# Optimization experiments

Hardware: AMD Instinct MI355X
Metric: run time of the kernel (lower is better)

## Reference

```python
import jax, jax.numpy as jnp
import numpy as np
import math

B, S, D, H, DFF = 4, 1024, 1024, 16, 4096
DK = D // H
EPS = 1e-5


def setup_inputs() -> dict:
    key = jax.random.key(0)
    ks = jax.random.split(key, 20)
    n = lambda k, shp: jax.random.normal(k, shp, jnp.float32) * 0.02
    inp = {
        "x": jax.random.normal(ks[0], (B, S, D), jnp.float32),
        "enc_output": jax.random.normal(ks[1], (B, S, D), jnp.float32),
        # source_mask is unused by the module's forward; target_mask is causal
        "source_mask": jnp.ones((B, 1, 1, S), jnp.int32),
        "target_mask": jnp.tril(jnp.ones((1, 1, S, S), jnp.int32)),
        # self-attention (torch Linear: y = x @ W.T + b)
        "sa_wq": n(ks[2], (D, D)), "sa_bq": jnp.zeros((D,), jnp.float32),
        "sa_wk": n(ks[3], (D, D)), "sa_bk": jnp.zeros((D,), jnp.float32),
        "sa_wv": n(ks[4], (D, D)), "sa_bv": jnp.zeros((D,), jnp.float32),
        "sa_wo": n(ks[5], (D, D)), "sa_bo": jnp.zeros((D,), jnp.float32),
        # cross-attention (nn.MultiheadAttention packed in_proj)
        "ca_in_w": n(ks[6], (3 * D, D)), "ca_in_b": jnp.zeros((3 * D,), jnp.float32),
        "ca_out_w": n(ks[7], (D, D)), "ca_out_b": jnp.zeros((D,), jnp.float32),
        # feed-forward
        "ff_w1": n(ks[8], (DFF, D)), "ff_b1": jnp.zeros((DFF,), jnp.float32),
        "ff_w2": n(ks[9], (D, DFF)), "ff_b2": jnp.zeros((D,), jnp.float32),
        # layer norms
        "n1_g": jnp.ones((D,), jnp.float32), "n1_b": jnp.zeros((D,), jnp.float32),
        "n2_g": jnp.ones((D,), jnp.float32), "n2_b": jnp.zeros((D,), jnp.float32),
        "n3_g": jnp.ones((D,), jnp.float32), "n3_b": jnp.zeros((D,), jnp.float32),
    }
    return inp


def _layernorm(x, g, b):
    m = jnp.mean(x, axis=-1, keepdims=True)
    v = jnp.var(x, axis=-1, keepdims=True)
    return (x - m) * jax.lax.rsqrt(v + EPS) * g + b


def _split_heads(t):  # [B,L,D] -> [B,H,L,DK]
    Bb, L, _ = t.shape
    return t.reshape(Bb, L, H, DK).transpose(0, 2, 1, 3)


def _attn(q, k, v, mask):
    # q,k,v: [B,H,Lq/ Lk, DK]
    scores = jnp.einsum("bhqd,bhkd->bhqk", q, k) / math.sqrt(DK)
    if mask is not None:
        scores = jnp.where(mask == 0, jnp.float32(-1e9), scores)
    probs = jax.nn.softmax(scores, axis=-1)
    out = jnp.einsum("bhqk,bhkd->bhqd", probs, v)  # [B,H,Lq,DK]
    Bb, _, Lq, _ = out.shape
    return out.transpose(0, 2, 1, 3).reshape(Bb, Lq, D)


def reference(x, enc_output, source_mask, target_mask,
              sa_wq, sa_bq, sa_wk, sa_bk, sa_wv, sa_bv, sa_wo, sa_bo,
              ca_in_w, ca_in_b, ca_out_w, ca_out_b,
              ff_w1, ff_b1, ff_w2, ff_b2,
              n1_g, n1_b, n2_g, n2_b, n3_g, n3_b):
    # --- masked causal self-attention (hand-rolled MultiHeadAttention) ---
    q = _split_heads(x @ sa_wq.T + sa_bq)
    k = _split_heads(x @ sa_wk.T + sa_bk)
    v = _split_heads(x @ sa_wv.T + sa_bv)
    sa = _attn(q, k, v, target_mask) @ sa_wo.T + sa_bo
    x = _layernorm(x + sa, n1_g, n1_b)  # dropout p=0 -> identity

    # --- cross-attention (nn.MultiheadAttention, batch_first, no mask) ---
    wq, wk, wv = ca_in_w[:D], ca_in_w[D:2 * D], ca_in_w[2 * D:]
    bq, bk, bv = ca_in_b[:D], ca_in_b[D:2 * D], ca_in_b[2 * D:]
    q = _split_heads(x @ wq.T + bq)
    k = _split_heads(enc_output @ wk.T + bk)
    v = _split_heads(enc_output @ wv.T + bv)
    ca = _attn(q, k, v, None) @ ca_out_w.T + ca_out_b
    x = _layernorm(x + ca, n2_g, n2_b)

    # --- feed-forward ---
    ff = jax.nn.relu(x @ ff_w1.T + ff_b1) @ ff_w2.T + ff_b2
    x = _layernorm(x + ff, n3_g, n3_b)
    return x
```

## Files before the change

kernel.cpp:

```cpp
#include <hip/hip_runtime.h>
#include <hip/hip_bf16.h>
#include <stdint.h>
#include <math.h>

#define DEV static __device__ __forceinline__

typedef short bf16x8 __attribute__((ext_vector_type(8)));
typedef float f32x4 __attribute__((ext_vector_type(4)));
typedef float f32x16 __attribute__((ext_vector_type(16)));
typedef unsigned short u16;

static constexpr int Sq   = 1024;
static constexpr int Dm   = 1024;
static constexpr int Hh   = 16;
static constexpr int Mrows = 4096;
static constexpr int DFFn = 4096;


DEV u16 f2bf(float f) {
    union { float f; unsigned u; } c; c.f = f;
    unsigned u = c.u;
    return (u16)((u + 0x7FFFu + ((u >> 16) & 1u)) >> 16);
}

DEV float bf2f(u16 v) {
    union { unsigned u; float f; } c; c.u = ((unsigned)v) << 16; return c.f;
}

DEV unsigned cvt_pk_bf16(float lo, float hi) {
    unsigned r;
    asm("v_cvt_pk_bf16_f32 %0, %1, %2" : "=v"(r) : "v"(lo), "v"(hi));
    return r;
}

DEV float fast_exp2(float x) {
#if __has_builtin(__builtin_amdgcn_exp2f)
    return __builtin_amdgcn_exp2f(x);
#else
    float r; asm("v_exp_f32 %0, %1" : "=v"(r) : "v"(x)); return r;
#endif
}

DEV void gload_lds16(void* lds, const void* g) {
    using gvp = __attribute__((address_space(1))) void*;
    using lvp = __attribute__((address_space(3))) void*;
    __builtin_amdgcn_global_load_lds((gvp)const_cast<void*>(g), (lvp)lds, 16, 0, 0);
}

DEV int swz64(int L) { return L ^ (((L >> 7) & 7) << 4); }


__global__ __launch_bounds__(256) void cast_multi_kernel(
    const float* s0, const float* s1, const float* s2, const float* s3, const float* s4,
    const float* s5, const float* s6, const float* s7, const float* s8, const float* s9,
    u16* d0, u16* d1, u16* d2, u16* d3, u16* d4,
    u16* d5, u16* d6, u16* d7, u16* d8, u16* d9,
    int e0, int e1, int e2, int e3, int e4,
    int e5, int e6, int e7, int e8, int e9)
{
    int i = blockIdx.x * 256 + threadIdx.x;
    if (i >= e9) return;
    const float* s; u16* d; int b;
    if      (i < e0) { s = s0; d = d0; b = 0;  }
    else if (i < e1) { s = s1; d = d1; b = e0; }
    else if (i < e2) { s = s2; d = d2; b = e1; }
    else if (i < e3) { s = s3; d = d3; b = e2; }
    else if (i < e4) { s = s4; d = d4; b = e3; }
    else if (i < e5) { s = s5; d = d5; b = e4; }
    else if (i < e6) { s = s6; d = d6; b = e5; }
    else if (i < e7) { s = s7; d = d7; b = e6; }
    else if (i < e8) { s = s8; d = d8; b = e7; }
    else             { s = s9; d = d9; b = e8; }
    int j = i - b;
    float4 v = ((const float4*)s)[j];
    ushort4 o;
    o.x = f2bf(v.x); o.y = f2bf(v.y); o.z = f2bf(v.z); o.w = f2bf(v.w);
    ((ushort4*)d)[j] = o;
}


template<int MODE, int BSPLIT>
__global__ __launch_bounds__(512) void gemm256_kernel(
    const u16* __restrict__ A, const u16* __restrict__ W,
    const float* __restrict__ bias0, const float* __restrict__ bias1,
    const float* __restrict__ bias2,
    void* __restrict__ Cout,
    void* __restrict__ P1, void* __restrict__ P2, void* __restrict__ P3,
    int N, int ldK, int Kpass)
{
    __shared__ char ldsA[65536];
    __shared__ char ldsB[65536];
    const int tid = threadIdx.x;
    const int w = tid >> 6, l = tid & 63;
    const int lr = l & 15, lg = l >> 4;
    const int wr = w >> 2, wc = w & 3;

    const int nwg = gridDim.x * gridDim.y;
    const int lin = blockIdx.y * gridDim.x + blockIdx.x;
    const int swz = (lin & 7) * (nwg >> 3) + (lin >> 3);
    const size_t tm = (size_t)(swz / gridDim.x) * 256;
    const size_t tn = (size_t)(swz % gridDim.x) * 256;
    const size_t kz = (size_t)blockIdx.z * Kpass;

    int offA[8], offB[4];
    #pragma unroll
    for (int m = 0; m < 8; ++m)
        offA[m] = swz64((wr * 128 + m * 16 + lr) * 64 + lg * 16);
    #pragma unroll
    for (int n = 0; n < 4; ++n)
        offB[n] = swz64((wc * 64 + n * 16 + lr) * 64 + lg * 16);

    const int Ls = swz64(tid * 16);
    const int sr = Ls >> 6, scc = Ls & 63;
    const size_t ldb = (size_t)ldK * 2;
    const char* aS = (const char*)A + (tm + sr) * ldb + kz * 2 + scc;
    const char* bS = (const char*)W + (tn + sr) * ldb + kz * 2 + scc;

    auto AH = [&](int b, int h) -> char* { return ldsA + (b * 2 + h) * 16384; };
    auto BH = [&](int b, int h) -> char* { return ldsB + (b * 2 + h) * 16384; };
    auto stage = [&](char* half, const char* src) {
        gload_lds16(half + w * 1024, src);
        gload_lds16(half + 8192 + w * 1024, src + 128 * ldb);
    };

    const int nt = Kpass >> 6;
    const int niter = nt >> 1;

    f32x4 acc[8][4] = {};
    bf16x8 bq[4];

    stage(AH(0, 0), aS);        stage(BH(0, 0), bS);
    stage(AH(0, 1), aS + 64);   stage(BH(0, 1), bS + 64);
    stage(AH(1, 0), aS + 128);  stage(BH(1, 0), bS + 128);
    asm volatile("s_waitcnt vmcnt(4)" ::: "memory");
    __builtin_amdgcn_s_barrier();

    for (int it = 0; it < niter; ++it) {
        const int t0 = it * 2;
        const bool last = (it == niter - 1);
        #pragma unroll
        for (int p = 0; p < 8; ++p) {
            const int ts = p >> 2;
            const int kk = (p >> 1) & 1, mh = p & 1;

            if (mh == 0) {
                #pragma unroll
                for (int n = 0; n < 4; ++n)
                    bq[n] = *(const bf16x8*)(BH(ts, kk) + offB[n]);
            }
            bf16x8 aF[4];
            #pragma unroll
            for (int q = 0; q < 4; ++q)
                aF[q] = *(const bf16x8*)(AH(ts, kk) + offA[mh * 4 + q]);

            if (p == 0)      { stage(AH(1, 1), aS + (size_t)(t0 + 1) * 128 + 64); }
            else if (p == 1) { stage(BH(1, 1), bS + (size_t)(t0 + 1) * 128 + 64); }
            else if (p == 2) { if (t0 + 2 < nt) stage(AH(0, 0), aS + (size_t)(t0 + 2) * 128); }
            else if (p == 3) { if (t0 + 2 < nt) stage(BH(0, 0), bS + (size_t)(t0 + 2) * 128); }
            else if (p == 4) { if (t0 + 2 < nt) stage(AH(0, 1), aS + (size_t)(t0 + 2) * 128 + 64); }
            else if (p == 5) { if (t0 + 2 < nt) stage(BH(0, 1), bS + (size_t)(t0 + 2) * 128 + 64); }
            else if (p == 6) { if (t0 + 3 < nt) stage(AH(1, 0), aS + (size_t)(t0 + 3) * 128); }
            else             { if (t0 + 3 < nt) stage(BH(1, 0), bS + (size_t)(t0 + 3) * 128); }

            if (p == 3) {
                if (last) asm volatile("s_waitcnt vmcnt(0)" ::: "memory");
                else      asm volatile("s_waitcnt vmcnt(4)" ::: "memory");
            } else if (p == 7 && !last) {
                asm volatile("s_waitcnt vmcnt(4)" ::: "memory");
            }
            __builtin_amdgcn_s_barrier();
            asm volatile("s_waitcnt lgkmcnt(0)");
            __builtin_amdgcn_sched_barrier(0);
            __builtin_amdgcn_s_setprio(1);
            #pragma unroll
            for (int q = 0; q < 4; ++q)
                #pragma unroll
                for (int n = 0; n < 4; ++n)
                    acc[mh * 4 + q][n] = __builtin_amdgcn_mfma_f32_16x16x32_bf16(
                        aF[q], bq[n], acc[mh * 4 + q][n], 0, 0, 0);
            __builtin_amdgcn_s_setprio(0);
        }
    }

    u16* Pp = nullptr;
    float bv[4];
    if (MODE == 3) {
        Pp = (u16*)((blockIdx.z == 0) ? Cout : (blockIdx.z == 1) ? P1 : (blockIdx.z == 2) ? P2 : P3);
    } else {
        #pragma unroll
        for (int n = 0; n < 4; ++n) {
            const int col = (int)tn + wc * 64 + n * 16 + lr;
            if (BSPLIT) {
                const float* bp = (col < 1024) ? bias0 : (col < 2048) ? bias1 : bias2;
                bv[n] = bp[col & 1023];
            } else {
                bv[n] = bias0[col];
            }
        }
    }
    #pragma unroll
    for (int m = 0; m < 8; ++m) {
        #pragma unroll
        for (int n = 0; n < 4; ++n) {
            const size_t col = tn + wc * 64 + n * 16 + lr;
            #pragma unroll
            for (int j = 0; j < 4; ++j) {
                const size_t row = tm + wr * 128 + m * 16 + lg * 4 + j;
                if (MODE == 3) {
                    Pp[row * (size_t)N + col] = f2bf(acc[m][n][j]);
                } else {
                    float v = acc[m][n][j] + bv[n];
                    if (MODE == 2) v = fmaxf(v, 0.f);
                    ((u16*)Cout)[row * (size_t)N + col] = f2bf(v);
                }
            }
        }
    }
}


template<int OUT_BF16, int RELU>
__global__ __launch_bounds__(256, 3) void gemm_bt64_kernel(
    const u16* __restrict__ A, const u16* __restrict__ W,
    const float* __restrict__ bias, void* __restrict__ Cout,
    int N, int K)
{
    __shared__ char Ald[2][8192];
    __shared__ char Bld[2][16384];
    const int tid = threadIdx.x;
    const int w  = tid >> 6, l = tid & 63;
    const int lr = l & 15,  lg = l >> 4;

    const int nwg = gridDim.x * gridDim.y;
    const int lin = blockIdx.y * gridDim.x + blockIdx.x;
    const int swz = (lin & 7) * (nwg >> 3) + (lin >> 3);
    const size_t tm = (size_t)(swz / gridDim.x) * 64;
    const size_t tn = (size_t)(swz % gridDim.x) * 128;

    const int Ls = swz64(tid * 16);
    const int sr = Ls >> 7, sc = (Ls & 127) >> 1;
    const u16* As = A + (tm + sr) * (size_t)K + sc;
    const u16* Bs = W + (tn + sr) * (size_t)K + sc;
    const int woff = w * 1024;

    auto stage = [&](int b, int k0) {
        gload_lds16(Ald[b] + woff,         As + k0);
        gload_lds16(Ald[b] + 4096 + woff,  As + (size_t)32 * K + k0);
        gload_lds16(Bld[b] + woff,         Bs + k0);
        gload_lds16(Bld[b] + 4096 + woff,  Bs + (size_t)32 * K + k0);
        gload_lds16(Bld[b] + 8192 + woff,  Bs + (size_t)64 * K + k0);
        gload_lds16(Bld[b] + 12288 + woff, Bs + (size_t)96 * K + k0);
    };

    int offA[4][2], offB[2][2];
    #pragma unroll
    for (int m = 0; m < 4; ++m)
        #pragma unroll
        for (int kk = 0; kk < 2; ++kk)
            offA[m][kk] = swz64((m * 16 + lr) * 128 + kk * 64 + lg * 16);
    #pragma unroll
    for (int n = 0; n < 2; ++n)
        #pragma unroll
        for (int kk = 0; kk < 2; ++kk)
            offB[n][kk] = swz64((w * 32 + n * 16 + lr) * 128 + kk * 64 + lg * 16);

    f32x4 acc[4][2] = {};
    const int nt = K >> 6;

    stage(0, 0);
    asm volatile("s_waitcnt vmcnt(0)" ::: "memory");
    __syncthreads();

    for (int t = 0; t < nt; ++t) {
        const int cur = t & 1;
        if (t + 1 < nt) stage(cur ^ 1, (t + 1) * 64);
        #pragma unroll
        for (int kk = 0; kk < 2; ++kk) {
            bf16x8 aF[4], bq[2];
            #pragma unroll
            for (int m = 0; m < 4; ++m) aF[m] = *(const bf16x8*)(Ald[cur] + offA[m][kk]);
            #pragma unroll
            for (int n = 0; n < 2; ++n) bq[n] = *(const bf16x8*)(Bld[cur] + offB[n][kk]);
            asm volatile("s_waitcnt lgkmcnt(0)");
            __builtin_amdgcn_sched_barrier(0);
            __builtin_amdgcn_s_setprio(1);
            #pragma unroll
            for (int m = 0; m < 4; ++m)
                #pragma unroll
                for (int n = 0; n < 2; ++n)
                    acc[m][n] = __builtin_amdgcn_mfma_f32_16x16x32_bf16(aF[m], bq[n], acc[m][n], 0, 0, 0);
            __builtin_amdgcn_s_setprio(0);
        }
        if (t + 1 < nt) asm volatile("s_waitcnt vmcnt(0)" ::: "memory");
        __syncthreads();
    }

    float bv[2];
    #pragma unroll
    for (int n = 0; n < 2; ++n) bv[n] = bias[tn + w * 32 + n * 16 + lr];

    #pragma unroll
    for (int m = 0; m < 4; ++m) {
        #pragma unroll
        for (int n = 0; n < 2; ++n) {
            const size_t col = tn + w * 32 + n * 16 + lr;
            #pragma unroll
            for (int j = 0; j < 4; ++j) {
                const size_t row = tm + m * 16 + lg * 4 + j;
                float v = acc[m][n][j] + bv[n];
                if (RELU) v = fmaxf(v, 0.f);
                if (OUT_BF16) ((u16*)Cout)[row * (size_t)N + col] = f2bf(v);
                else          ((float*)Cout)[row * (size_t)N + col] = v;
            }
        }
    }
}


template<int CAUSAL>
__global__ __launch_bounds__(512, 2) void attn_kernel(
    const u16* __restrict__ Qm, int ldq,
    const u16* __restrict__ Km, int ldk,
    const u16* __restrict__ Vm, int ldv,
    u16* __restrict__ Om)
{
    __shared__ char lds[33280];

    const int tid = threadIdx.x;
    const int w = tid >> 6, l = tid & 63;
    const int lq = l & 31, hi = l >> 5;
    const int s = w & 3, hfk = w >> 2;
    const int bh = blockIdx.x;
    const int b = bh >> 4, h = bh & 15;
    const int q0 = (CAUSAL ? (gridDim.y - 1 - blockIdx.y) : blockIdx.y) * 128;
    const int qw0 = q0 + s * 32;
    const size_t baseQ = (size_t)b * Sq * ldq + (size_t)h * 64;
    const size_t baseK = (size_t)b * Sq * ldk + (size_t)h * 64;
    const size_t baseV = (size_t)b * Sq * ldv + (size_t)h * 64;
    const size_t baseO = (size_t)b * Sq * Dm  + (size_t)h * 64;

    const int qrow = qw0 + lq;
    bf16x8 bq[4];
    #pragma unroll
    for (int kc = 0; kc < 4; ++kc)
        bq[kc] = *(const bf16x8*)&Qm[baseQ + (size_t)qrow * ldq + kc * 16 + hi * 8];

    const int tl = tid & 255, pstg = tid >> 8;
    const int kr  = tl >> 2;
    const int kcB = (tl & 3) * 32;
    const int vdg = tl >> 5;
    const int vkp = tl & 31;
    char* Kst = lds + pstg * 8192;
    char* Vst = lds + 16384 + pstg * 8192;
    const char* Kb_ = lds + hfk * 8192;
    const char* Vb_ = lds + 16384 + hfk * 8192;

    f32x16 o0 = {}, o1 = {};
    float lj = 0.f;

    const int nt_blk  = CAUSAL ? ((q0 + 128) >> 6) : (Sq >> 6);
    const int nrounds = nt_blk >> 1;
    const float cexp = 0.125f * 1.44269504f;
    const float CSH  = 10.0f;

    uint4 kaA, kbA, vaA, vbA, kaB, kbB, vaB, vbB;
    auto loadKV = [&](int rv, uint4& ka, uint4& kb, uint4& va, uint4& vb) {
        const int kv = (rv * 2 + pstg) << 6;
        ka = *(const uint4*)&Km[baseK + (size_t)(kv + kr) * ldk + kcB / 2];
        kb = *(const uint4*)&Km[baseK + (size_t)(kv + kr) * ldk + kcB / 2 + 8];
        va = *(const uint4*)&Vm[baseV + (size_t)(kv + vkp * 2    ) * ldv + vdg * 8];
        vb = *(const uint4*)&Vm[baseV + (size_t)(kv + vkp * 2 + 1) * ldv + vdg * 8];
    };

    loadKV(0, kaA, kbA, vaA, vbA);
    if (nrounds > 1) loadKV(1, kaB, kbB, vaB, vbB);

    for (int r = 0; r < nrounds; ++r) {
        {
            const int sk = (kr & 7) << 4;
            *(uint4*)(Kst + kr * 128 + ((kcB     ) ^ sk)) = kaA;
            *(uint4*)(Kst + kr * 128 + ((kcB + 16) ^ sk)) = kbA;
            const u16* pa_ = (const u16*)&vaA;
            const u16* pb_ = (const u16*)&vbA;
            #pragma unroll
            for (int i = 0; i < 8; ++i) {
                const int d = vdg * 8 + i;
                unsigned val = (unsigned)pa_[i] | ((unsigned)pb_[i] << 16);
                *(unsigned*)(Vst + d * 128 + ((vkp * 4) ^ ((d & 7) << 4))) = val;
            }
        }
        __syncthreads();
        if (r + 2 < nrounds) loadKV(r + 2, kaA, kbA, vaA, vbA);

        const int kv0 = (r * 2 + hfk) << 6;
        if (!CAUSAL || kv0 < qw0 + 32) {
            const int skq = (lq & 7) << 4;

            f32x16 sv[2] = {};
            #pragma unroll
            for (int n = 0; n < 2; ++n) {
                const int rowb = (n * 32 + lq) * 128;
                #pragma unroll
                for (int kc = 0; kc < 4; ++kc) {
                    bf16x8 kf = *(const bf16x8*)(Kb_ + rowb + ((kc * 32 + hi * 16) ^ skq));
                    sv[n] = __builtin_amdgcn_mfma_f32_32x32x16_bf16(kf, bq[kc], sv[n], 0, 0, 0);
                }
            }

            const bool diag = CAUSAL && (kv0 + 63 > qw0);
            float rs0 = 0.f, rs1 = 0.f;
            #pragma unroll
            for (int n = 0; n < 2; ++n)
                #pragma unroll
                for (int r2 = 0; r2 < 16; ++r2) {
                    float v = sv[n][r2];
                    if (diag) {
                        int key = kv0 + n * 32 + (r2 & 3) + 8 * (r2 >> 2) + 4 * hi;
                        if (key > qrow) v = -3.0e8f;
                    }
                    float e = fast_exp2(fmaf(v, cexp, -CSH));
                    sv[n][r2] = e;
                    if (r2 & 1) rs1 += e; else rs0 += e;
                }
            float rs = rs0 + rs1;
            rs += __shfl_xor(rs, 32);
            lj += rs;

            unsigned wv[2][8];
            #pragma unroll
            for (int n = 0; n < 2; ++n)
                #pragma unroll
                for (int m = 0; m < 8; ++m)
                    wv[n][m] = cvt_pk_bf16(sv[n][2 * m], sv[n][2 * m + 1]);

            #pragma unroll
            for (int ks = 0; ks < 4; ++ks) {
                const int n = ks >> 1, q_ = (ks & 1) * 4;
                unsigned r0 = (unsigned)__shfl_xor((int)wv[n][q_ + 0], 32);
                unsigned r1 = (unsigned)__shfl_xor((int)wv[n][q_ + 1], 32);
                unsigned r2w = (unsigned)__shfl_xor((int)wv[n][q_ + 2], 32);
                unsigned r3 = (unsigned)__shfl_xor((int)wv[n][q_ + 3], 32);
                union { unsigned u[4]; bf16x8 v; } pa;
                pa.u[0] = hi ? r2w          : wv[n][q_ + 0];
                pa.u[1] = hi ? r3           : wv[n][q_ + 1];
                pa.u[2] = hi ? wv[n][q_ + 2] : r0;
                pa.u[3] = hi ? wv[n][q_ + 3] : r1;
                const int koff = (ks * 32 + hi * 16);
                bf16x8 vf0 = *(const bf16x8*)(Vb_ + lq * 128        + (koff ^ skq));
                bf16x8 vf1 = *(const bf16x8*)(Vb_ + (32 + lq) * 128 + (koff ^ skq));
                o0 = __builtin_amdgcn_mfma_f32_32x32x16_bf16(pa.v, vf0, o0, 0, 0, 0);
                o1 = __builtin_amdgcn_mfma_f32_32x32x16_bf16(pa.v, vf1, o1, 0, 0, 0);
            }
        }
        __syncthreads();

        uint4 t;
        t = kaA; kaA = kaB; kaB = t;
        t = kbA; kbA = kbB; kbB = t;
        t = vaA; vaA = vaB; vaB = t;
        t = vbA; vbA = vbB; vbB = t;
    }

    char* ob = lds + s * 8192 + l * 128;
    float* mlb = (float*)(lds + 32768) + s * 32 + lq;
    const int sko = (l & 7) << 4;

    if (hfk == 1) {
        #pragma unroll
        for (int i = 0; i < 4; ++i) {
            f32x4 t0v = { o0[4 * i], o0[4 * i + 1], o0[4 * i + 2], o0[4 * i + 3] };
            f32x4 t1v = { o1[4 * i], o1[4 * i + 1], o1[4 * i + 2], o1[4 * i + 3] };
            *(f32x4*)(ob + ((i * 16) ^ sko))      = t0v;
            *(f32x4*)(ob + ((64 + i * 16) ^ sko)) = t1v;
        }
        if (hi == 0) mlb[0] = lj;
    }
    __syncthreads();
    if (hfk == 0) {
        const float linv = __builtin_amdgcn_rcpf(lj + mlb[0]);
        f32x4 b0[4], b1[4];
        #pragma unroll
        for (int i = 0; i < 4; ++i) {
            b0[i] = *(const f32x4*)(ob + ((i * 16) ^ sko));
            b1[i] = *(const f32x4*)(ob + ((64 + i * 16) ^ sko));
        }
        #pragma unroll
        for (int r2 = 0; r2 < 16; ++r2) {
            const int crow = (r2 & 3) + 8 * (r2 >> 2) + 4 * hi;
            const float lr_ = __shfl(linv, crow);
            const size_t rowoff = baseO + (size_t)(qw0 + crow) * Dm;
            float v0 = (o0[r2] + b0[r2 >> 2][r2 & 3]) * lr_;
            float v1 = (o1[r2] + b1[r2 >> 2][r2 & 3]) * lr_;
            Om[rowoff + lq]      = f2bf(v0);
            Om[rowoff + 32 + lq] = f2bf(v1);
        }
    }
}


__global__ __launch_bounds__(256) void add_ln_kernel(
    const float* __restrict__ A, const float* __restrict__ Bv,
    const float* __restrict__ g, const float* __restrict__ be,
    float* __restrict__ Y, u16* __restrict__ Ybf)
{
    const int row = blockIdx.x;
    const int tid = threadIdx.x;
    const size_t off = (size_t)row * Dm;
    float4 a4 = ((const float4*)(A + off))[tid];
    float4 b4 = ((const float4*)(Bv + off))[tid];
    float4 xv;
    xv.x = a4.x + b4.x; xv.y = a4.y + b4.y; xv.z = a4.z + b4.z; xv.w = a4.w + b4.w;
    float s = xv.x + xv.y + xv.z + xv.w;
    float q = xv.x * xv.x + xv.y * xv.y + xv.z * xv.z + xv.w * xv.w;
    #pragma unroll
    for (int m = 1; m < 64; m <<= 1) {
        s += __shfl_xor(s, m);
        q += __shfl_xor(q, m);
    }
    __shared__ float ss[4], qq[4];
    if ((tid & 63) == 0) { ss[tid >> 6] = s; qq[tid >> 6] = q; }
    __syncthreads();
    s = ss[0] + ss[1] + ss[2] + ss[3];
    q = qq[0] + qq[1] + qq[2] + qq[3];
    const float mean = s * (1.f / 1024.f);
    const float var  = q * (1.f / 1024.f) - mean * mean;
    const float rstd = rsqrtf(var + 1e-5f);
    float4 g4  = ((const float4*)g)[tid];
    float4 be4 = ((const float4*)be)[tid];
    float4 y;
    y.x = (xv.x - mean) * rstd * g4.x + be4.x;
    y.y = (xv.y - mean) * rstd * g4.y + be4.y;
    y.z = (xv.z - mean) * rstd * g4.z + be4.z;
    y.w = (xv.w - mean) * rstd * g4.w + be4.w;
    ((float4*)(Y + off))[tid] = y;
    if (Ybf) {
        ushort4 ob;
        ob.x = f2bf(y.x); ob.y = f2bf(y.y); ob.z = f2bf(y.z); ob.w = f2bf(y.w);
        ((ushort4*)(Ybf + off))[tid] = ob;
    }
}


__global__ __launch_bounds__(256) void add_ln_red4_kernel(
    const float* __restrict__ X,
    const u16* __restrict__ P0, const u16* __restrict__ P1,
    const u16* __restrict__ P2, const u16* __restrict__ P3,
    const float* __restrict__ bias,
    const float* __restrict__ g, const float* __restrict__ be,
    float* __restrict__ Y)
{
    const int row = blockIdx.x;
    const int tid = threadIdx.x;
    const size_t off = (size_t)row * Dm;
    float4 a4 = ((const float4*)(X + off))[tid];
    ushort4 u0 = ((const ushort4*)(P0 + off))[tid];
    ushort4 u1 = ((const ushort4*)(P1 + off))[tid];
    ushort4 u2 = ((const ushort4*)(P2 + off))[tid];
    ushort4 u3 = ((const ushort4*)(P3 + off))[tid];
    float4 b4 = ((const float4*)bias)[tid];
    float4 xv;
    xv.x = a4.x + bf2f(u0.x) + bf2f(u1.x) + bf2f(u2.x) + bf2f(u3.x) + b4.x;
    xv.y = a4.y + bf2f(u0.y) + bf2f(u1.y) + bf2f(u2.y) + bf2f(u3.y) + b4.y;
    xv.z = a4.z + bf2f(u0.z) + bf2f(u1.z) + bf2f(u2.z) + bf2f(u3.z) + b4.z;
    xv.w = a4.w + bf2f(u0.w) + bf2f(u1.w) + bf2f(u2.w) + bf2f(u3.w) + b4.w;
    float s = xv.x + xv.y + xv.z + xv.w;
    float q = xv.x * xv.x + xv.y * xv.y + xv.z * xv.z + xv.w * xv.w;
    #pragma unroll
    for (int m = 1; m < 64; m <<= 1) {
        s += __shfl_xor(s, m);
        q += __shfl_xor(q, m);
    }
    __shared__ float ss[4], qq[4];
    if ((tid & 63) == 0) { ss[tid >> 6] = s; qq[tid >> 6] = q; }
    __syncthreads();
    s = ss[0] + ss[1] + ss[2] + ss[3];
    q = qq[0] + qq[1] + qq[2] + qq[3];
    const float mean = s * (1.f / 1024.f);
    const float var  = q * (1.f / 1024.f) - mean * mean;
    const float rstd = rsqrtf(var + 1e-5f);
    float4 g4  = ((const float4*)g)[tid];
    float4 be4 = ((const float4*)be)[tid];
    float4 y;
    y.x = (xv.x - mean) * rstd * g4.x + be4.x;
    y.y = (xv.y - mean) * rstd * g4.y + be4.y;
    y.z = (xv.z - mean) * rstd * g4.z + be4.z;
    y.w = (xv.w - mean) * rstd * g4.w + be4.w;
    ((float4*)(Y + off))[tid] = y;
}


extern "C" void kernel_launch(void* const* d_in, const int* in_sizes, int n_in,
                              void* d_out, int out_size, void* d_ws, size_t ws_size,
                              hipStream_t stream)
{
    const float* x       = (const float*)d_in[0];
    const float* enc     = (const float*)d_in[1];
    const float* sa_wq   = (const float*)d_in[4];
    const float* sa_bq   = (const float*)d_in[5];
    const float* sa_wk   = (const float*)d_in[6];
    const float* sa_bk   = (const float*)d_in[7];
    const float* sa_wv   = (const float*)d_in[8];
    const float* sa_bv   = (const float*)d_in[9];
    const float* sa_wo   = (const float*)d_in[10];
    const float* sa_bo   = (const float*)d_in[11];
    const float* ca_in_w = (const float*)d_in[12];
    const float* ca_in_b = (const float*)d_in[13];
    const float* ca_out_w= (const float*)d_in[14];
    const float* ca_out_b= (const float*)d_in[15];
    const float* ff_w1   = (const float*)d_in[16];
    const float* ff_b1   = (const float*)d_in[17];
    const float* ff_w2   = (const float*)d_in[18];
    const float* ff_b2   = (const float*)d_in[19];
    const float* n1_g = (const float*)d_in[20];
    const float* n1_b = (const float*)d_in[21];
    const float* n2_g = (const float*)d_in[22];
    const float* n2_b = (const float*)d_in[23];
    const float* n3_g = (const float*)d_in[24];
    const float* n3_b = (const float*)d_in[25];

    char* p = (char*)d_ws;
    auto take = [&](size_t bytes) -> char* {
        char* r = p; p += (bytes + 255) & ~(size_t)255; return r;
    };
    const size_t MDbf = (size_t)Mrows * Dm * 2;
    const size_t MDf  = (size_t)Mrows * Dm * 4;
    const size_t DD   = (size_t)Dm * Dm;

    u16* xb     = (u16*)take(MDbf);
    u16* encb   = (u16*)take(MDbf);
    u16* wqkv   = (u16*)take(3 * DD * 2);
    u16* wob    = (u16*)take(DD * 2);
    u16* cainb  = (u16*)take(3 * DD * 2);
    u16* caoutb = (u16*)take(DD * 2);
    u16* fw1b   = (u16*)take((size_t)DFFn * Dm * 2);
    u16* fw2b   = (u16*)take((size_t)Dm * DFFn * 2);
    u16* SCR    = (u16*)take((size_t)Mrows * DFFn * 2);
    u16* AOb    = (u16*)take(MDbf);
    float* tmpf = (float*)take(MDf);
    float* x1f  = (float*)take(MDf);
    u16*   x1b  = (u16*)take(MDbf);
    float* x2f  = (float*)take(MDf);
    u16*   x2b  = (u16*)take(MDbf);
    if ((size_t)(p - (char*)d_ws) > ws_size) return;

    u16* fp0 = AOb;
    u16* fp1 = (u16*)tmpf;
    u16* fp2 = (u16*)tmpf + 4 * 1024 * 1024;
    u16* fp3 = xb;

    {
        const int sx  = (int)((size_t)Mrows * Dm / 4);
        const int sw  = (int)(DD / 4);
        const int e0 = sx;
        const int e1 = e0 + sx;
        const int e2 = e1 + sw;
        const int e3 = e2 + sw;
        const int e4 = e3 + sw;
        const int e5 = e4 + sw;
        const int e6 = e5 + 3 * sw;
        const int e7 = e6 + sw;
        const int e8 = e7 + 4 * sw;
        const int e9 = e8 + 4 * sw;
        cast_multi_kernel<<<dim3((e9 + 255) / 256), dim3(256), 0, stream>>>(
            x, enc, sa_wq, sa_wk, sa_wv, sa_wo, ca_in_w, ca_out_w, ff_w1, ff_w2,
            xb, encb, wqkv, wqkv + DD, wqkv + 2 * DD, wob, cainb, caoutb, fw1b, fw2b,
            e0, e1, e2, e3, e4, e5, e6, e7, e8, e9);
    }

    const dim3 blk(256);
    const dim3 blk512(512);
    const size_t M4 = (size_t)Mrows * Dm;

    gemm256_kernel<1, 1><<<dim3(12, 16), blk512, 0, stream>>>(
        xb, wqkv, sa_bq, sa_bk, sa_bv, (void*)SCR, nullptr, nullptr, nullptr, 3072, Dm, Dm);
    attn_kernel<1><<<dim3(4 * Hh, Sq / 128), blk512, 0, stream>>>(SCR, 3072, SCR + 1024, 3072, SCR + 2048, 3072, AOb);
    gemm_bt64_kernel<0, 0><<<dim3(Dm / 128, Mrows / 64), blk, 0, stream>>>(AOb, wob, sa_bo, (void*)tmpf, Dm, Dm);
    add_ln_kernel<<<dim3(Mrows), blk, 0, stream>>>(x, tmpf, n1_g, n1_b, x1f, x1b);

    u16* Qc  = SCR;
    u16* KVc = SCR + M4;
    gemm_bt64_kernel<1, 0><<<dim3(Dm / 128, Mrows / 64), blk, 0, stream>>>(x1b, cainb, ca_in_b, (void*)Qc, Dm, Dm);
    gemm256_kernel<1, 1><<<dim3(8, 16), blk512, 0, stream>>>(
        encb, cainb + DD, ca_in_b + Dm, ca_in_b + 2 * Dm, ca_in_b + 2 * Dm,
        (void*)KVc, nullptr, nullptr, nullptr, 2048, Dm, Dm);
    attn_kernel<0><<<dim3(4 * Hh, Sq / 128), blk512, 0, stream>>>(Qc, 1024, KVc, 2048, KVc + 1024, 2048, AOb);
    gemm_bt64_kernel<0, 0><<<dim3(Dm / 128, Mrows / 64), blk, 0, stream>>>(AOb, caoutb, ca_out_b, (void*)tmpf, Dm, Dm);
    add_ln_kernel<<<dim3(Mrows), blk, 0, stream>>>(x1f, tmpf, n2_g, n2_b, x2f, x2b);

    u16* ffh = SCR;
    gemm256_kernel<2, 0><<<dim3(16, 16), blk512, 0, stream>>>(
        x2b, fw1b, ff_b1, ff_b1, ff_b1, (void*)ffh, nullptr, nullptr, nullptr, DFFn, Dm, Dm);
    gemm256_kernel<3, 0><<<dim3(4, 16, 4), blk512, 0, stream>>>(
        ffh, fw2b, nullptr, nullptr, nullptr, (void*)fp0, (void*)fp1, (void*)fp2, (void*)fp3, Dm, DFFn, 1024);
    add_ln_red4_kernel<<<dim3(Mrows), blk, 0, stream>>>(x2f, fp0, fp1, fp2, fp3, ff_b2, n3_g, n3_b, (float*)d_out);
}
```

Before: 305.4 us.

## Double-buffer K/V tiles in LDS for attention to drop one barrier per round

```diff
diff --git a/kernel.cpp b/kernel.cpp
--- a/kernel.cpp
+++ b/kernel.cpp
@@ -324,7 +324,7 @@
     const u16* __restrict__ Vm, int ldv,
     u16* __restrict__ Om)
 {
-    __shared__ char lds[33280];
+    __shared__ char lds[66048];
 
     const int tid = threadIdx.x;
     const int w = tid >> 6, l = tid & 63;
@@ -350,10 +350,6 @@
     const int kcB = (tl & 3) * 32;
     const int vdg = tl >> 5;
     const int vkp = tl & 31;
-    char* Kst = lds + pstg * 8192;
-    char* Vst = lds + 16384 + pstg * 8192;
-    const char* Kb_ = lds + hfk * 8192;
-    const char* Vb_ = lds + 16384 + hfk * 8192;
 
     f32x16 o0 = {}, o1 = {};
     float lj = 0.f;
@@ -363,40 +359,46 @@
     const float cexp = 0.125f * 1.44269504f;
     const float CSH  = 10.0f;
 
-    uint4 kaA, kbA, vaA, vbA, kaB, kbB, vaB, vbB;
-    auto loadKV = [&](int rv, uint4& ka, uint4& kb, uint4& va, uint4& vb) {
+    uint4 ka, kb, va, vb;
+    auto loadKV = [&](int rv) {
         const int kv = (rv * 2 + pstg) << 6;
         ka = *(const uint4*)&Km[baseK + (size_t)(kv + kr) * ldk + kcB / 2];
         kb = *(const uint4*)&Km[baseK + (size_t)(kv + kr) * ldk + kcB / 2 + 8];
         va = *(const uint4*)&Vm[baseV + (size_t)(kv + vkp * 2    ) * ldv + vdg * 8];
         vb = *(const uint4*)&Vm[baseV + (size_t)(kv + vkp * 2 + 1) * ldv + vdg * 8];
     };
-
-    loadKV(0, kaA, kbA, vaA, vbA);
-    if (nrounds > 1) loadKV(1, kaB, kbB, vaB, vbB);
+    auto stageTo = [&](int bsel) {
+        char* Kst = lds + bsel * 32768 + pstg * 8192;
+        char* Vst = lds + bsel * 32768 + 16384 + pstg * 8192;
+        const int sk = (kr & 7) << 4;
+        *(uint4*)(Kst + kr * 128 + ((kcB     ) ^ sk)) = ka;
+        *(uint4*)(Kst + kr * 128 + ((kcB + 16) ^ sk)) = kb;
+        const u16* pa_ = (const u16*)&va;
+        const u16* pb_ = (const u16*)&vb;
+        #pragma unroll
+        for (int i = 0; i < 8; ++i) {
+            const int d = vdg * 8 + i;
+            unsigned val = (unsigned)pa_[i] | ((unsigned)pb_[i] << 16);
+            *(unsigned*)(Vst + d * 128 + ((vkp * 4) ^ ((d & 7) << 4))) = val;
+        }
+    };
+
+    loadKV(0);
+    stageTo(0);
+    loadKV(1);
+    __syncthreads();
 
     for (int r = 0; r < nrounds; ++r) {
-        {
-            const int sk = (kr & 7) << 4;
-            *(uint4*)(Kst + kr * 128 + ((kcB     ) ^ sk)) = kaA;
-            *(uint4*)(Kst + kr * 128 + ((kcB + 16) ^ sk)) = kbA;
-            const u16* pa_ = (const u16*)&vaA;
-            const u16* pb_ = (const u16*)&vbA;
-            #pragma unroll
-            for (int i = 0; i < 8; ++i) {
-                const int d = vdg * 8 + i;
-                unsigned val = (unsigned)pa_[i] | ((unsigned)pb_[i] << 16);
-                *(unsigned*)(Vst + d * 128 + ((vkp * 4) ^ ((d & 7) << 4))) = val;
-            }
-        }
-        __syncthreads();
-        if (r + 2 < nrounds) loadKV(r + 2, kaA, kbA, vaA, vbA);
-
+        const int rp = r & 1;
+        const char* Kb_ = lds + rp * 32768 + hfk * 8192;
+        const char* Vb_ = lds + rp * 32768 + 16384 + hfk * 8192;
         const int kv0 = (r * 2 + hfk) << 6;
-        if (!CAUSAL || kv0 < qw0 + 32) {
-            const int skq = (lq & 7) << 4;
-
-            f32x16 sv[2] = {};
+        const bool docmp = (!CAUSAL || kv0 < qw0 + 32);
+        const int skq = (lq & 7) << 4;
+
+        f32x16 sv[2];
+        if (docmp) {
+            sv[0] = (f32x16){}; sv[1] = (f32x16){};
             #pragma unroll
             for (int n = 0; n < 2; ++n) {
                 const int rowb = (n * 32 + lq) * 128;
@@ -406,7 +408,12 @@
                     sv[n] = __builtin_amdgcn_mfma_f32_32x32x16_bf16(kf, bq[kc], sv[n], 0, 0, 0);
                 }
             }
-
+        }
+
+        if (r + 1 < nrounds) stageTo(rp ^ 1);
+        if (r + 2 < nrounds) loadKV(r + 2);
+
+        if (docmp) {
             const bool diag = CAUSAL && (kv0 + 63 > qw0);
             float rs0 = 0.f, rs1 = 0.f;
             #pragma unroll
@@ -441,8 +448,8 @@
                 unsigned r2w = (unsigned)__shfl_xor((int)wv[n][q_ + 2], 32);
                 unsigned r3 = (unsigned)__shfl_xor((int)wv[n][q_ + 3], 32);
                 union { unsigned u[4]; bf16x8 v; } pa;
-                pa.u[0] = hi ? r2w          : wv[n][q_ + 0];
-                pa.u[1] = hi ? r3           : wv[n][q_ + 1];
+                pa.u[0] = hi ? r2w           : wv[n][q_ + 0];
+                pa.u[1] = hi ? r3            : wv[n][q_ + 1];
                 pa.u[2] = hi ? wv[n][q_ + 2] : r0;
                 pa.u[3] = hi ? wv[n][q_ + 3] : r1;
                 const int koff = (ks * 32 + hi * 16);
@@ -453,16 +460,10 @@
             }
         }
         __syncthreads();
-
-        uint4 t;
-        t = kaA; kaA = kaB; kaB = t;
-        t = kbA; kbA = kbB; kbB = t;
-        t = vaA; vaA = vaB; vaB = t;
-        t = vbA; vbA = vbB; vbB = t;
     }
 
     char* ob = lds + s * 8192 + l * 128;
-    float* mlb = (float*)(lds + 32768) + s * 32 + lq;
+    float* mlb = (float*)(lds + 65536) + s * 32 + lq;
     const int sko = (l & 7) << 4;
 
     if (hfk == 1) {
```

Measured after the change: 302.8 us. Within noise of the previous version (-0.9%).
